# Performance work log

Measured on AMD Instinct MI355X. Metric: run time of the kernel, lower is better.

## Reference

```python
import jax, jax.numpy as jnp
import numpy as np

DIM = 768
HEADS = 12
HEAD_DIM = DIM // HEADS
SCALE = HEAD_DIM ** -0.5
B, N = 64, 196


def rel_indices(n):
    # Same construction as get_rel_indices: channel 0 = indx, channel 1 = indy
    img = int(n ** 0.5)
    ind = jnp.arange(img)[None, :] - jnp.arange(img)[:, None]      # (img, img)
    indx = jnp.tile(ind, (img, img))                                # (N, N)
    indy = jnp.repeat(jnp.repeat(ind, img, axis=0), img, axis=1)    # (N, N)
    return jnp.stack([indx, indy], axis=-1).astype(jnp.float32)     # (N, N, 2)


def setup_inputs() -> dict:
    key = jax.random.key(0)
    ks = jax.random.split(key, 9)
    std = 0.02
    return {
        "x": jax.random.normal(ks[0], (B, N, DIM), dtype=jnp.float32),
        "qk_w": jax.random.normal(ks[1], (2 * DIM, DIM), dtype=jnp.float32) * std,
        "v_w": jax.random.normal(ks[2], (DIM, DIM), dtype=jnp.float32) * std,
        "w1_w": jax.random.normal(ks[3], (DIM, 2), dtype=jnp.float32) * std,
        "w1_b": jnp.zeros((DIM,), dtype=jnp.float32),
        "w2": jax.random.normal(ks[4], (DIM, 1), dtype=jnp.float32) * std,
        "b2": jnp.ones((HEADS,), dtype=jnp.float32),
        "proj_w": jax.random.normal(ks[5], (DIM, DIM), dtype=jnp.float32) * std,
        "proj_b": jnp.zeros((DIM,), dtype=jnp.float32),
    }


def reference(x, qk_w, v_w, w1_w, w1_b, w2, b2, proj_w, proj_b):
    Bx, Nx, C = x.shape
    rel = rel_indices(Nx)                                           # (N, N, 2)

    # qk projection -> q, k of shape (B, H, N, hd)
    qk = (x @ qk_w.T).reshape(Bx, Nx, 2, HEADS, HEAD_DIM)
    q = qk[:, :, 0].transpose(0, 2, 1, 3)
    k = qk[:, :, 1].transpose(0, 2, 1, 3)

    # learned relative-position bias: MLP(rel) -> per-head scalar map
    pos_emb = jax.nn.relu(rel @ w1_w.T + w1_b)                      # (N, N, dim)
    pos_emb = pos_emb.reshape(Nx, Nx, HEADS, HEAD_DIM)
    pos_map = jnp.einsum('ijhm,hm->ijh', pos_emb, w2.reshape(HEADS, HEAD_DIM)) + b2  # (N,N,H)

    # attention scores, modulated multiplicatively by the position map
    score = jnp.einsum('bhnd,bhmd->bhnm', q, k) * SCALE             # (B, H, N, N)
    score = score * pos_map.transpose(2, 0, 1)[None]                # broadcast over B
    attn = jax.nn.softmax(score, axis=-1)

    v = (x @ v_w.T).reshape(Bx, Nx, HEADS, HEAD_DIM).transpose(0, 2, 1, 3)
    out = jnp.einsum('bhnm,bhmd->bhnd', attn, v)                    # (B, H, N, hd)
    out = out.transpose(0, 2, 1, 3).reshape(Bx, Nx, C)
    return out @ proj_w.T + proj_b
```

## Files before the change

kernel.cpp:

```cpp
#include <hip/hip_runtime.h>

#define NTOK 196
#define NHEAD 12
#define HDIM 64
#define CDIM 768
#define BSZ 64
#define MROWS (BSZ * NTOK)
#define PART_STRIDE 9633792
#define BH_STRIDE 12544
#define VT_LD 224
#define VT_BH (HDIM * VT_LD)
#define PM_H (NTOK * NTOK)
#define P_LD 232

typedef __bf16 bf16x8 __attribute__((ext_vector_type(8)));
typedef float f32x4 __attribute__((ext_vector_type(4)));

static __device__ __forceinline__ unsigned short f_to_bf16(float f) {
    union { float f; unsigned int i; } v; v.f = f;
    unsigned int x = v.i;
    unsigned int r = x + 0x7fffu + ((x >> 16) & 1u);
    return (unsigned short)(r >> 16);
}

static __device__ __forceinline__ void gld16(const unsigned short* g, unsigned short* l) {
    __builtin_amdgcn_global_load_lds(
        (__attribute__((address_space(1))) void*)(unsigned long long)(const void*)g,
        (__attribute__((address_space(3))) void*)(unsigned int)(unsigned long long)(void*)l,
        16, 0, 0);
}

__global__ void cvt_f32_bf16(const float* __restrict__ src,
                             unsigned short* __restrict__ dst, int n4) {
    int i = blockIdx.x * 256 + threadIdx.x;
    if (i >= n4) return;
    float4 v = ((const float4*)src)[i];
    ushort4 o;
    o.x = f_to_bf16(v.x); o.y = f_to_bf16(v.y);
    o.z = f_to_bf16(v.z); o.w = f_to_bf16(v.w);
    ((ushort4*)dst)[i] = o;
}

__global__ void pos_kernel(const float* __restrict__ w1,
                           const float* __restrict__ w1b,
                           const float* __restrict__ w2,
                           const float* __restrict__ b2,
                           float* __restrict__ pm2) {
    int idx = blockIdx.x * 256 + threadIdx.x;
    if (idx >= NHEAD * NTOK * NTOK) return;
    int h = idx / PM_H;
    int r = idx - h * PM_H;
    int i = r / NTOK;
    int j = r - i * NTOK;
    float rx = (float)(j % 14 - i % 14);
    float ry = (float)(j / 14 - i / 14);
    float acc = 0.f;
    int base = h * HDIM;
    #pragma unroll 8
    for (int t = 0; t < HDIM; ++t) {
        int c = base + t;
        float e = rx * w1[2 * c] + ry * w1[2 * c + 1] + w1b[c];
        e = e > 0.f ? e : 0.f;
        acc += e * w2[c];
    }
    pm2[idx] = (acc + b2[h]) * 0.125f;
}

template <int MODE>
__global__ __launch_bounds__(256) void gemm_qkv_t(
        const unsigned short* __restrict__ A,
        const unsigned short* __restrict__ W,
        unsigned short* __restrict__ qkv,
        int n0base) {
    __shared__ __align__(16) unsigned short As[2][128 * 32];
    __shared__ __align__(16) unsigned short Bs[2][128 * 32];
    int tid = threadIdx.x;
    int m0 = blockIdx.y * 128;
    int n0 = n0base + blockIdx.x * 128;
    int w = tid >> 6, lane = tid & 63, l15 = lane & 15, quad = lane >> 4;
    int mw = (w & 1) * 64, nw = (w >> 1) * 64;

    const unsigned short* ga = A + (size_t)(m0 + (tid >> 2)) * CDIM + (tid & 3) * 8;
    const unsigned short* gb = W + (size_t)(n0 + (tid >> 2)) * CDIM + (tid & 3) * 8;

    f32x4 acc[4][4];
    #pragma unroll
    for (int i = 0; i < 4; ++i)
        #pragma unroll
        for (int j = 0; j < 4; ++j) acc[i][j] = (f32x4){0.f, 0.f, 0.f, 0.f};

    auto issue = [&](int buf) {
        gld16(ga, &As[buf][tid * 8]);
        gld16(ga + 64 * CDIM, &As[buf][2048 + tid * 8]);
        gld16(gb, &Bs[buf][tid * 8]);
        gld16(gb + 64 * CDIM, &Bs[buf][2048 + tid * 8]);
        ga += 32; gb += 32;
    };
    auto compute = [&](int buf) {
        bf16x8 af[4], bf[4];
        #pragma unroll
        for (int mt = 0; mt < 4; ++mt)
            af[mt] = *(const bf16x8*)&As[buf][(mw + mt * 16 + l15) * 32 + quad * 8];
        #pragma unroll
        for (int nt = 0; nt < 4; ++nt)
            bf[nt] = *(const bf16x8*)&Bs[buf][(nw + nt * 16 + l15) * 32 + quad * 8];
        #pragma unroll
        for (int mt = 0; mt < 4; ++mt)
            #pragma unroll
            for (int nt = 0; nt < 4; ++nt) {
                if (MODE == 0)
                    acc[mt][nt] = __builtin_amdgcn_mfma_f32_16x16x32_bf16(bf[nt], af[mt], acc[mt][nt], 0, 0, 0);
                else
                    acc[mt][nt] = __builtin_amdgcn_mfma_f32_16x16x32_bf16(af[mt], bf[nt], acc[mt][nt], 0, 0, 0);
            }
    };

    issue(0);
    #pragma unroll 1
    for (int kt = 0; kt < 24; kt += 2) {
        __syncthreads();
        issue(1);
        compute(0);
        __syncthreads();
        if (kt + 2 < 24) issue(0);
        compute(1);
    }

    if (MODE == 0) {
        int part = (n0 >= CDIM) ? 1 : 0;
        const size_t pbase = (size_t)part * PART_STRIDE;
        int cb = n0 + nw + quad * 4 - part * CDIM;
        #pragma unroll
        for (int mt = 0; mt < 4; ++mt) {
            int m = m0 + mw + mt * 16 + l15;
            int b = m / NTOK, n = m - b * NTOK;
            size_t base_m = pbase + (size_t)b * NHEAD * BH_STRIDE + n * HDIM;
            #pragma unroll
            for (int nt = 0; nt < 4; ++nt) {
                int c = cb + nt * 16;
                int h = c >> 6, d = c & 63;
                uint2 pv;
                pv.x = (unsigned int)f_to_bf16(acc[mt][nt][0]) |
                       ((unsigned int)f_to_bf16(acc[mt][nt][1]) << 16);
                pv.y = (unsigned int)f_to_bf16(acc[mt][nt][2]) |
                       ((unsigned int)f_to_bf16(acc[mt][nt][3]) << 16);
                *(uint2*)(qkv + base_m + (size_t)h * BH_STRIDE + d) = pv;
            }
        }
    } else {
        #pragma unroll
        for (int mt = 0; mt < 4; ++mt) {
            int m = m0 + mw + mt * 16 + quad * 4;
            int b = m / NTOK, n = m - b * NTOK;
            size_t base_m = (size_t)2 * PART_STRIDE + (size_t)b * NHEAD * VT_BH + n;
            #pragma unroll
            for (int nt = 0; nt < 4; ++nt) {
                int c = n0 + nw + nt * 16 + l15 - 3 * 512;
                int h = c >> 6, d = c & 63;
                uint2 pv;
                pv.x = (unsigned int)f_to_bf16(acc[mt][nt][0]) |
                       ((unsigned int)f_to_bf16(acc[mt][nt][1]) << 16);
                pv.y = (unsigned int)f_to_bf16(acc[mt][nt][2]) |
                       ((unsigned int)f_to_bf16(acc[mt][nt][3]) << 16);
                *(uint2*)(qkv + base_m + (size_t)h * VT_BH + d * VT_LD) = pv;
            }
        }
    }
}

__global__ __launch_bounds__(64) void attn_mfma(
        const unsigned short* __restrict__ qkv,
        const float* __restrict__ pm2,
        unsigned short* __restrict__ attn_out) {
    __shared__ __align__(16) unsigned short P[16 * P_LD];
    int t = blockIdx.x;
    int bh = blockIdx.y;
    int b = bh / NHEAD, h = bh - b * NHEAD;
    int lane = threadIdx.x;
    int l15 = lane & 15, quad = lane >> 4;

    #pragma unroll
    for (int z = 0; z < 8; ++z) {
        int e = z * 64 + lane;
        P[(e >> 5) * P_LD + 196 + (e & 31)] = 0;
    }

    const unsigned short* qbase = qkv + (size_t)bh * BH_STRIDE;
    const unsigned short* kbase = qkv + (size_t)PART_STRIDE + (size_t)bh * BH_STRIDE;
    const unsigned short* vbase = qkv + (size_t)2 * PART_STRIDE + (size_t)bh * VT_BH;
    const float* pmh = pm2 + (size_t)h * PM_H;

    int qrow = t * 16 + l15; if (qrow > 195) qrow = 195;
    bf16x8 aq0 = *(const bf16x8*)(qbase + qrow * HDIM + quad * 8);
    bf16x8 aq1 = *(const bf16x8*)(qbase + qrow * HDIM + 32 + quad * 8);

    f32x4 s[13];
    #pragma unroll
    for (int nt = 0; nt < 13; ++nt) s[nt] = (f32x4){0.f, 0.f, 0.f, 0.f};
    #pragma unroll
    for (int nt = 0; nt < 13; ++nt) {
        int krow = nt * 16 + l15; if (krow > 195) krow = 195;
        bf16x8 b0 = *(const bf16x8*)(kbase + krow * HDIM + quad * 8);
        bf16x8 b1 = *(const bf16x8*)(kbase + krow * HDIM + 32 + quad * 8);
        s[nt] = __builtin_amdgcn_mfma_f32_16x16x32_bf16(aq0, b0, s[nt], 0, 0, 0);
        s[nt] = __builtin_amdgcn_mfma_f32_16x16x32_bf16(aq1, b1, s[nt], 0, 0, 0);
    }

    float rsum[4] = {0.f, 0.f, 0.f, 0.f};
    int irow[4];
    #pragma unroll
    for (int r = 0; r < 4; ++r) {
        int i = t * 16 + quad * 4 + r; if (i > 195) i = 195;
        irow[r] = i;
    }
    #pragma unroll
    for (int nt = 0; nt < 13; ++nt) {
        int j = nt * 16 + l15;
        bool valid = (j < 196);
        int jc = valid ? j : 195;
        #pragma unroll
        for (int r = 0; r < 4; ++r) {
            float pmv = pmh[irow[r] * NTOK + jc];
            float p = __expf(s[nt][r] * pmv);
            p = valid ? p : 0.f;
            rsum[r] += p;
            P[(quad * 4 + r) * P_LD + nt * 16 + l15] = f_to_bf16(p);
        }
    }
    float inv[4];
    #pragma unroll
    for (int r = 0; r < 4; ++r) {
        float v = rsum[r];
        v += __shfl_xor(v, 1); v += __shfl_xor(v, 2);
        v += __shfl_xor(v, 4); v += __shfl_xor(v, 8);
        inv[r] = 1.f / v;
    }

    f32x4 o[4];
    #pragma unroll
    for (int dt = 0; dt < 4; ++dt) o[dt] = (f32x4){0.f, 0.f, 0.f, 0.f};
    #pragma unroll
    for (int kk = 0; kk < 7; ++kk) {
        bf16x8 ap = *(const bf16x8*)&P[l15 * P_LD + kk * 32 + quad * 8];
        #pragma unroll
        for (int dt = 0; dt < 4; ++dt) {
            bf16x8 bv = *(const bf16x8*)(vbase + (dt * 16 + l15) * VT_LD + kk * 32 + quad * 8);
            o[dt] = __builtin_amdgcn_mfma_f32_16x16x32_bf16(ap, bv, o[dt], 0, 0, 0);
        }
    }

    #pragma unroll
    for (int r = 0; r < 4; ++r) {
        int row = t * 16 + quad * 4 + r;
        if (row < 196) {
            unsigned short* dst = attn_out + ((size_t)(b * NTOK + row)) * CDIM + h * HDIM + l15;
            #pragma unroll
            for (int dt = 0; dt < 4; ++dt)
                dst[dt * 16] = f_to_bf16(o[dt][r] * inv[r]);
        }
    }
}

__global__ __launch_bounds__(256) void gemm_proj(
        const unsigned short* __restrict__ A,
        const unsigned short* __restrict__ W,
        const float* __restrict__ bias,
        float* __restrict__ out) {
    __shared__ __align__(16) unsigned short As[2][128 * 32];
    __shared__ __align__(16) unsigned short Bs[2][128 * 32];
    int tid = threadIdx.x;
    int m0 = blockIdx.y * 128;
    int n0 = blockIdx.x * 128;
    int w = tid >> 6, lane = tid & 63, l15 = lane & 15, quad = lane >> 4;
    int mw = (w & 1) * 64, nw = (w >> 1) * 64;

    const unsigned short* ga = A + (size_t)(m0 + (tid >> 2)) * CDIM + (tid & 3) * 8;
    const unsigned short* gb = W + (size_t)(n0 + (tid >> 2)) * CDIM + (tid & 3) * 8;

    f32x4 acc[4][4];
    #pragma unroll
    for (int i = 0; i < 4; ++i)
        #pragma unroll
        for (int j = 0; j < 4; ++j) acc[i][j] = (f32x4){0.f, 0.f, 0.f, 0.f};

    auto issue = [&](int buf) {
        gld16(ga, &As[buf][tid * 8]);
        gld16(ga + 64 * CDIM, &As[buf][2048 + tid * 8]);
        gld16(gb, &Bs[buf][tid * 8]);
        gld16(gb + 64 * CDIM, &Bs[buf][2048 + tid * 8]);
        ga += 32; gb += 32;
    };
    auto compute = [&](int buf) {
        bf16x8 af[4], bf[4];
        #pragma unroll
        for (int mt = 0; mt < 4; ++mt)
            af[mt] = *(const bf16x8*)&As[buf][(mw + mt * 16 + l15) * 32 + quad * 8];
        #pragma unroll
        for (int nt = 0; nt < 4; ++nt)
            bf[nt] = *(const bf16x8*)&Bs[buf][(nw + nt * 16 + l15) * 32 + quad * 8];
        #pragma unroll
        for (int mt = 0; mt < 4; ++mt)
            #pragma unroll
            for (int nt = 0; nt < 4; ++nt)
                acc[mt][nt] = __builtin_amdgcn_mfma_f32_16x16x32_bf16(bf[nt], af[mt], acc[mt][nt], 0, 0, 0);
    };

    issue(0);
    #pragma unroll 1
    for (int kt = 0; kt < 24; kt += 2) {
        __syncthreads();
        issue(1);
        compute(0);
        __syncthreads();
        if (kt + 2 < 24) issue(0);
        compute(1);
    }

    #pragma unroll
    for (int nt = 0; nt < 4; ++nt) {
        int c = n0 + nw + nt * 16 + quad * 4;
        float4 bv = *(const float4*)(bias + c);
        #pragma unroll
        for (int mt = 0; mt < 4; ++mt) {
            int m = m0 + mw + mt * 16 + l15;
            float4 ov;
            ov.x = acc[mt][nt][0] + bv.x;
            ov.y = acc[mt][nt][1] + bv.y;
            ov.z = acc[mt][nt][2] + bv.z;
            ov.w = acc[mt][nt][3] + bv.w;
            *(float4*)(out + (size_t)m * CDIM + c) = ov;
        }
    }
}

extern "C" void kernel_launch(void* const* d_in, const int* in_sizes, int n_in,
                              void* d_out, int out_size, void* d_ws, size_t ws_size,
                              hipStream_t stream) {
    const float* x      = (const float*)d_in[0];
    const float* qk_w   = (const float*)d_in[1];
    const float* v_w    = (const float*)d_in[2];
    const float* w1_w   = (const float*)d_in[3];
    const float* w1_b   = (const float*)d_in[4];
    const float* w2     = (const float*)d_in[5];
    const float* b2     = (const float*)d_in[6];
    const float* proj_w = (const float*)d_in[7];
    const float* proj_b = (const float*)d_in[8];
    float* out = (float*)d_out;

    unsigned short* x_bf  = (unsigned short*)d_ws;
    unsigned short* w_cat = x_bf + 9633792;
    unsigned short* pw_bf = w_cat + 1769472;
    float* pm2            = (float*)(pw_bf + 589824);
    unsigned short* qkv   = (unsigned short*)(pm2 + 460992);
    unsigned short* attn_o = x_bf;

    cvt_f32_bf16<<<9408, 256, 0, stream>>>(x, x_bf, 2408448);
    cvt_f32_bf16<<<1152, 256, 0, stream>>>(qk_w, w_cat, 294912);
    cvt_f32_bf16<<<576, 256, 0, stream>>>(v_w, w_cat + 1179648, 147456);
    cvt_f32_bf16<<<576, 256, 0, stream>>>(proj_w, pw_bf, 147456);
    pos_kernel<<<1801, 256, 0, stream>>>(w1_w, w1_b, w2, b2, pm2);

    dim3 gqk(12, 98);
    gemm_qkv_t<0><<<gqk, 256, 0, stream>>>(x_bf, w_cat, qkv, 0);
    dim3 gv(6, 98);
    gemm_qkv_t<1><<<gv, 256, 0, stream>>>(x_bf, w_cat, qkv, 1536);

    dim3 ga(13, 768);
    attn_mfma<<<ga, 64, 0, stream>>>(qkv, pm2, attn_o);

    dim3 g2(6, 98);
    gemm_proj<<<g2, 256, 0, stream>>>(attn_o, pw_bf, proj_b, out);
}
```

Before: 330.6 us.

## Stage K in LDS per head and process query tiles with four waves

Result: slower. 345.1 us (+4.4%).

```diff
diff --git a/kernel.cpp b/kernel.cpp
--- a/kernel.cpp
+++ b/kernel.cpp
@@ -11,7 +11,8 @@
 #define VT_LD 224
 #define VT_BH (HDIM * VT_LD)
 #define PM_H (NTOK * NTOK)
-#define P_LD 232
+#define P_LD 224
+#define K2_HALF 6272
 
 typedef __bf16 bf16x8 __attribute__((ext_vector_type(8)));
 typedef float f32x4 __attribute__((ext_vector_type(4)));
@@ -134,7 +135,6 @@
         for (int mt = 0; mt < 4; ++mt) {
             int m = m0 + mw + mt * 16 + l15;
             int b = m / NTOK, n = m - b * NTOK;
-            size_t base_m = pbase + (size_t)b * NHEAD * BH_STRIDE + n * HDIM;
             #pragma unroll
             for (int nt = 0; nt < 4; ++nt) {
                 int c = cb + nt * 16;
@@ -144,7 +144,13 @@
                        ((unsigned int)f_to_bf16(acc[mt][nt][1]) << 16);
                 pv.y = (unsigned int)f_to_bf16(acc[mt][nt][2]) |
                        ((unsigned int)f_to_bf16(acc[mt][nt][3]) << 16);
-                *(uint2*)(qkv + base_m + (size_t)h * BH_STRIDE + d) = pv;
+                size_t idx;
+                if (part == 0)
+                    idx = (size_t)(b * NHEAD + h) * BH_STRIDE + n * HDIM + d;
+                else
+                    idx = pbase + (size_t)(b * NHEAD + h) * BH_STRIDE +
+                          (d >> 5) * K2_HALF + n * 32 + (d & 31);
+                *(uint2*)(qkv + idx) = pv;
             }
         }
     } else {
@@ -168,95 +174,103 @@
     }
 }
 
-__global__ __launch_bounds__(64) void attn_mfma(
+__global__ __launch_bounds__(256, 3) void attn_mfma(
         const unsigned short* __restrict__ qkv,
         const float* __restrict__ pm2,
         unsigned short* __restrict__ attn_out) {
-    __shared__ __align__(16) unsigned short P[16 * P_LD];
-    int t = blockIdx.x;
-    int bh = blockIdx.y;
+    __shared__ __align__(16) unsigned short Ks[2 * K2_HALF];
+    __shared__ __align__(16) unsigned short Pb[4][16 * P_LD];
+    int bh = blockIdx.x;
     int b = bh / NHEAD, h = bh - b * NHEAD;
-    int lane = threadIdx.x;
+    int tid = threadIdx.x;
+    int w = tid >> 6, lane = tid & 63;
     int l15 = lane & 15, quad = lane >> 4;
-
-    #pragma unroll
-    for (int z = 0; z < 8; ++z) {
-        int e = z * 64 + lane;
-        P[(e >> 5) * P_LD + 196 + (e & 31)] = 0;
-    }
 
     const unsigned short* qbase = qkv + (size_t)bh * BH_STRIDE;
     const unsigned short* kbase = qkv + (size_t)PART_STRIDE + (size_t)bh * BH_STRIDE;
     const unsigned short* vbase = qkv + (size_t)2 * PART_STRIDE + (size_t)bh * VT_BH;
     const float* pmh = pm2 + (size_t)h * PM_H;
 
-    int qrow = t * 16 + l15; if (qrow > 195) qrow = 195;
-    bf16x8 aq0 = *(const bf16x8*)(qbase + qrow * HDIM + quad * 8);
-    bf16x8 aq1 = *(const bf16x8*)(qbase + qrow * HDIM + 32 + quad * 8);
-
-    f32x4 s[13];
     #pragma unroll
-    for (int nt = 0; nt < 13; ++nt) s[nt] = (f32x4){0.f, 0.f, 0.f, 0.f};
-    #pragma unroll
-    for (int nt = 0; nt < 13; ++nt) {
-        int krow = nt * 16 + l15; if (krow > 195) krow = 195;
-        bf16x8 b0 = *(const bf16x8*)(kbase + krow * HDIM + quad * 8);
-        bf16x8 b1 = *(const bf16x8*)(kbase + krow * HDIM + 32 + quad * 8);
-        s[nt] = __builtin_amdgcn_mfma_f32_16x16x32_bf16(aq0, b0, s[nt], 0, 0, 0);
-        s[nt] = __builtin_amdgcn_mfma_f32_16x16x32_bf16(aq1, b1, s[nt], 0, 0, 0);
-    }
-
-    float rsum[4] = {0.f, 0.f, 0.f, 0.f};
-    int irow[4];
-    #pragma unroll
-    for (int r = 0; r < 4; ++r) {
-        int i = t * 16 + quad * 4 + r; if (i > 195) i = 195;
-        irow[r] = i;
-    }
-    #pragma unroll
-    for (int nt = 0; nt < 13; ++nt) {
-        int j = nt * 16 + l15;
-        bool valid = (j < 196);
-        int jc = valid ? j : 195;
-        #pragma unroll
-        for (int r = 0; r < 4; ++r) {
-            float pmv = pmh[irow[r] * NTOK + jc];
-            float p = __expf(s[nt][r] * pmv);
-            p = valid ? p : 0.f;
-            rsum[r] += p;
-            P[(quad * 4 + r) * P_LD + nt * 16 + l15] = f_to_bf16(p);
-        }
-    }
-    float inv[4];
-    #pragma unroll
-    for (int r = 0; r < 4; ++r) {
-        float v = rsum[r];
-        v += __shfl_xor(v, 1); v += __shfl_xor(v, 2);
-        v += __shfl_xor(v, 4); v += __shfl_xor(v, 8);
-        inv[r] = 1.f / v;
-    }
-
-    f32x4 o[4];
-    #pragma unroll
-    for (int dt = 0; dt < 4; ++dt) o[dt] = (f32x4){0.f, 0.f, 0.f, 0.f};
-    #pragma unroll
-    for (int kk = 0; kk < 7; ++kk) {
-        bf16x8 ap = *(const bf16x8*)&P[l15 * P_LD + kk * 32 + quad * 8];
-        #pragma unroll
-        for (int dt = 0; dt < 4; ++dt) {
-            bf16x8 bv = *(const bf16x8*)(vbase + (dt * 16 + l15) * VT_LD + kk * 32 + quad * 8);
-            o[dt] = __builtin_amdgcn_mfma_f32_16x16x32_bf16(ap, bv, o[dt], 0, 0, 0);
-        }
-    }
-
-    #pragma unroll
-    for (int r = 0; r < 4; ++r) {
-        int row = t * 16 + quad * 4 + r;
-        if (row < 196) {
-            unsigned short* dst = attn_out + ((size_t)(b * NTOK + row)) * CDIM + h * HDIM + l15;
-            #pragma unroll
-            for (int dt = 0; dt < 4; ++dt)
-                dst[dt * 16] = f_to_bf16(o[dt][r] * inv[r]);
+    for (int r = 0; r < 7; ++r) {
+        int idx = r * 2048 + tid * 8;
+        if (idx < 2 * K2_HALF) gld16(kbase + idx, &Ks[idx]);
+    }
+    unsigned short* P = &Pb[w][0];
+    {
+        int row = lane >> 2, c = 208 + (lane & 3) * 4;
+        *(uint2*)&P[row * P_LD + c] = (uint2){0u, 0u};
+    }
+    __syncthreads();
+
+    #pragma unroll 1
+    for (int t = w; t < 13; t += 4) {
+        int qrow = t * 16 + l15; if (qrow > 195) qrow = 195;
+        bf16x8 aq0 = *(const bf16x8*)(qbase + qrow * HDIM + quad * 8);
+        bf16x8 aq1 = *(const bf16x8*)(qbase + qrow * HDIM + 32 + quad * 8);
+
+        f32x4 s[13];
+        #pragma unroll
+        for (int nt = 0; nt < 13; ++nt) s[nt] = (f32x4){0.f, 0.f, 0.f, 0.f};
+        #pragma unroll
+        for (int nt = 0; nt < 13; ++nt) {
+            int jc = nt * 16 + l15; if (jc > 195) jc = 195;
+            bf16x8 k0 = *(const bf16x8*)&Ks[jc * 32 + quad * 8];
+            bf16x8 k1 = *(const bf16x8*)&Ks[K2_HALF + jc * 32 + quad * 8];
+            s[nt] = __builtin_amdgcn_mfma_f32_16x16x32_bf16(k0, aq0, s[nt], 0, 0, 0);
+            s[nt] = __builtin_amdgcn_mfma_f32_16x16x32_bf16(k1, aq1, s[nt], 0, 0, 0);
+        }
+
+        float rsum = 0.f;
+        const float* pmrow = pmh + qrow * NTOK;
+        #pragma unroll
+        for (int nt = 0; nt < 13; ++nt) {
+            int jb = nt * 16 + quad * 4;
+            int jbl = jb > 192 ? 192 : jb;
+            float4 pmv = *(const float4*)(pmrow + jbl);
+            float p0 = __expf(s[nt][0] * pmv.x);
+            float p1 = __expf(s[nt][1] * pmv.y);
+            float p2 = __expf(s[nt][2] * pmv.z);
+            float p3 = __expf(s[nt][3] * pmv.w);
+            if (jb + 0 > 195) p0 = 0.f;
+            if (jb + 1 > 195) p1 = 0.f;
+            if (jb + 2 > 195) p2 = 0.f;
+            if (jb + 3 > 195) p3 = 0.f;
+            rsum += (p0 + p1) + (p2 + p3);
+            uint2 pk;
+            pk.x = (unsigned int)f_to_bf16(p0) | ((unsigned int)f_to_bf16(p1) << 16);
+            pk.y = (unsigned int)f_to_bf16(p2) | ((unsigned int)f_to_bf16(p3) << 16);
+            *(uint2*)&P[l15 * P_LD + jb] = pk;
+        }
+        rsum += __shfl_xor(rsum, 16);
+        rsum += __shfl_xor(rsum, 32);
+        float inv = 1.f / rsum;
+
+        f32x4 o[4];
+        #pragma unroll
+        for (int dt = 0; dt < 4; ++dt) o[dt] = (f32x4){0.f, 0.f, 0.f, 0.f};
+        #pragma unroll
+        for (int kk = 0; kk < 7; ++kk) {
+            bf16x8 pf = *(const bf16x8*)&P[l15 * P_LD + kk * 32 + quad * 8];
+            #pragma unroll
+            for (int dt = 0; dt < 4; ++dt) {
+                bf16x8 vv = *(const bf16x8*)(vbase + (dt * 16 + l15) * VT_LD + kk * 32 + quad * 8);
+                o[dt] = __builtin_amdgcn_mfma_f32_16x16x32_bf16(vv, pf, o[dt], 0, 0, 0);
+            }
+        }
+
+        int orow = t * 16 + l15;
+        if (orow < 196) {
+            unsigned short* dst = attn_out + ((size_t)(b * NTOK + orow)) * CDIM + h * HDIM + quad * 4;
+            #pragma unroll
+            for (int dt = 0; dt < 4; ++dt) {
+                uint2 ov;
+                ov.x = (unsigned int)f_to_bf16(o[dt][0] * inv) |
+                       ((unsigned int)f_to_bf16(o[dt][1] * inv) << 16);
+                ov.y = (unsigned int)f_to_bf16(o[dt][2] * inv) |
+                       ((unsigned int)f_to_bf16(o[dt][3] * inv) << 16);
+                *(uint2*)(dst + dt * 16) = ov;
+            }
         }
     }
 }
@@ -365,8 +379,7 @@
     dim3 gv(6, 98);
     gemm_qkv_t<1><<<gv, 256, 0, stream>>>(x_bf, w_cat, qkv, 1536);
 
-    dim3 ga(13, 768);
-    attn_mfma<<<ga, 64, 0, stream>>>(qkv, pm2, attn_o);
+    attn_mfma<<<768, 256, 0, stream>>>(qkv, pm2, attn_o);
 
     dim3 g2(6, 98);
     gemm_proj<<<g2, 256, 0, stream>>>(attn_o, pw_bf, proj_b, out);
```
